# Kernel tuning notes

Measured on AMD Instinct MI355X. Metric: run time of the kernel, lower is better.

## Reference

```python
import jax, jax.numpy as jnp
import numpy as np

N_NODES = 50000
N_GRAPHS = 64


def gcn_conv(x, W, b, src, dst, n_nodes):
    """PyG GCNConv: sym-normalized aggregation with self-loops.
    out_i = sum_{j->i} d_j^{-1/2} d_i^{-1/2} (x_j W) + b, self-loops included."""
    loops = jnp.arange(n_nodes, dtype=src.dtype)
    s = jnp.concatenate([src, loops])  # [E+N]
    d = jnp.concatenate([dst, loops])
    h = x @ W  # [N, H]
    deg = jax.ops.segment_sum(jnp.ones_like(s, dtype=h.dtype), d, num_segments=n_nodes)
    dinv = jnp.where(deg > 0, jax.lax.rsqrt(jnp.maximum(deg, 1.0)), 0.0)
    norm = dinv[s] * dinv[d]  # [E+N]
    msg = h[s] * norm[:, None]  # gather + scale, [E+N, H]
    out = jax.ops.segment_sum(msg, d, num_segments=n_nodes)  # scatter-add
    return out + b


def setup_inputs() -> dict:
    key = jax.random.key(0)
    k1, k2, k3, k4, k5, k6, k7, k8, k9 = jax.random.split(key, 9)
    in_dim, hid, num_robots, out_size = 16, 128, 8, 2
    x = jax.random.normal(k1, (N_NODES, in_dim), dtype=jnp.float32)
    edge_index = jax.random.randint(k2, (2, 800000), 0, N_NODES, dtype=jnp.int64)
    batch = jnp.sort(jax.random.randint(k3, (N_NODES,), 0, N_GRAPHS, dtype=jnp.int64))
    s1 = 1.0 / np.sqrt(in_dim)
    s2 = 1.0 / np.sqrt(hid)
    W1 = jax.random.uniform(k4, (in_dim, hid), jnp.float32, -s1, s1)
    b1 = jax.random.uniform(k5, (hid,), jnp.float32, -s1, s1)
    W2 = jax.random.uniform(k6, (hid, hid), jnp.float32, -s2, s2)
    b2 = jax.random.uniform(k7, (hid,), jnp.float32, -s2, s2)
    Wfc = jax.random.uniform(k8, (hid, out_size * num_robots), jnp.float32, -s2, s2)
    bfc = jax.random.uniform(k9, (out_size * num_robots,), jnp.float32, -s2, s2)
    return {"x": x, "edge_index": edge_index, "batch": batch,
            "W1": W1, "b1": b1, "W2": W2, "b2": b2, "Wfc": Wfc, "bfc": bfc}


def reference(x, edge_index, batch, W1, b1, W2, b2, Wfc, bfc):
    src, dst = edge_index[0], edge_index[1]
    n = x.shape[0]
    h = jax.nn.relu(gcn_conv(x, W1, b1, src, dst, n))
    h = jax.nn.relu(gcn_conv(h, W2, b2, src, dst, n))
    # global_mean_pool over graph ids
    sums = jax.ops.segment_sum(h, batch, num_segments=N_GRAPHS)  # [G, H]
    cnt = jax.ops.segment_sum(jnp.ones((n,), h.dtype), batch, num_segments=N_GRAPHS)
    pooled = sums / jnp.maximum(cnt, 1.0)[:, None]
    vel = pooled @ Wfc + bfc  # [G, num_robots*2]
    return vel.reshape(-1, 8, 2)
```

## Files before the change

### kernel.cpp

```cpp
#include <hip/hip_runtime.h>
#include <hip/hip_bf16.h>

#define HID 128
#define IN_DIM 16

typedef short bf16x8 __attribute__((ext_vector_type(8)));
typedef float f32x4 __attribute__((ext_vector_type(4)));
typedef unsigned short u16x8 __attribute__((ext_vector_type(8)));

__device__ __forceinline__ unsigned short f2bf(float f) {
    unsigned int u = __float_as_uint(f);
    unsigned int r = (u + 0x7FFFu + ((u >> 16) & 1u)) >> 16;
    return (unsigned short)r;
}
__device__ __forceinline__ float bf2f(unsigned short u) {
    return __uint_as_float(((unsigned int)u) << 16);
}

__global__ __launch_bounds__(256) void k_hist(const int* __restrict__ dst,
                                              int* __restrict__ hist,
                                              int E, int NB, int chunk) {
    __shared__ int lh[256];
    lh[threadIdx.x] = 0;
    __syncthreads();
    int s0 = blockIdx.x * chunk;
    int e_end = min(E, s0 + chunk);
    for (int e = s0 + threadIdx.x; e < e_end; e += 256)
        atomicAdd(&lh[dst[e] >> 8], 1);
    __syncthreads();
    for (int i = threadIdx.x; i < NB; i += 256)
        hist[blockIdx.x * NB + i] = lh[i];
}

__global__ __launch_bounds__(256) void k_hist_scan(int* __restrict__ hist,
                                                   int* __restrict__ btot, int NB) {
    __shared__ int sdata[256];
    int b = blockIdx.x, t = threadIdx.x;
    int v = hist[t * NB + b];
    sdata[t] = v;
    __syncthreads();
    for (int off = 1; off < 256; off <<= 1) {
        int tmp = (t >= off) ? sdata[t - off] : 0;
        __syncthreads();
        sdata[t] += tmp;
        __syncthreads();
    }
    hist[t * NB + b] = sdata[t] - v;
    if (t == 255) btot[b] = sdata[255];
}

__global__ __launch_bounds__(256) void k_misc(const int* __restrict__ btot,
                                              int* __restrict__ bucket_base,
                                              const int* __restrict__ batch, float* __restrict__ cnt,
                                              const float* __restrict__ W2,
                                              unsigned short* __restrict__ W2T,
                                              float* __restrict__ pooled,
                                              int N, int G, int NB, int E) {
    int bid = blockIdx.x;
    int t = threadIdx.x;
    if (bid == 0) {
        __shared__ int sdata[256];
        int v = (t < NB) ? btot[t] : 0;
        sdata[t] = v;
        __syncthreads();
        for (int off = 1; off < 256; off <<= 1) {
            int tmp = (t >= off) ? sdata[t - off] : 0;
            __syncthreads();
            sdata[t] += tmp;
            __syncthreads();
        }
        if (t < NB) bucket_base[t] = sdata[t] - v;
        if (t == 0) bucket_base[NB] = E;
    } else if (bid == 1) {
        int g = t;
        if (g >= G) return;
        int lo = 0, hi = N;
        while (lo < hi) { int mid = (lo + hi) >> 1; if (batch[mid] < g) lo = mid + 1; else hi = mid; }
        int start = lo;
        lo = 0; hi = N;
        while (lo < hi) { int mid = (lo + hi) >> 1; if (batch[mid] <= g) lo = mid + 1; else hi = mid; }
        cnt[g] = (float)(lo - start);
    } else if (bid < 66) {
        int i = (bid - 2) * 256 + t;
        int n = i >> 7, k = i & 127;
        W2T[i] = f2bf(W2[(size_t)k * HID + n]);
    } else {
        int i = (bid - 66) * 256 + t;
        if (i < G * HID) pooled[i] = 0.f;
    }
}

__global__ __launch_bounds__(256) void k_bucket(const int* __restrict__ src, const int* __restrict__ dst,
                                                const int* __restrict__ hist,
                                                const int* __restrict__ bucket_base,
                                                unsigned int* __restrict__ bucketed,
                                                int E, int NB, int chunk) {
    __shared__ int lcur[256];
    for (int i = threadIdx.x; i < NB; i += 256)
        lcur[i] = hist[blockIdx.x * NB + i] + bucket_base[i];
    __syncthreads();
    int s0 = blockIdx.x * chunk;
    int e_end = min(E, s0 + chunk);
    for (int e = s0 + threadIdx.x; e < e_end; e += 256) {
        int d = dst[e], s = src[e];
        int p = atomicAdd(&lcur[d >> 8], 1);
        bucketed[p] = ((unsigned int)(d & 255) << 16) | (unsigned int)s;
    }
}

__global__ __launch_bounds__(256) void k_fill3(const unsigned int* __restrict__ bucketed,
                                               const int* __restrict__ bucket_base,
                                               unsigned short* __restrict__ csr,
                                               int* __restrict__ offs,
                                               int* __restrict__ indeg,
                                               float* __restrict__ dinv, int N) {
    __shared__ int lh[256];
    __shared__ int sc[256];
    int b = blockIdx.x, t = threadIdx.x;
    int n0 = b << 8;
    lh[t] = 0;
    __syncthreads();
    int bb = bucket_base[b], be = bucket_base[b + 1];
    for (int e = bb + t; e < be; e += 256)
        atomicAdd(&lh[bucketed[e] >> 16], 1);
    __syncthreads();
    int deg = lh[t];
    sc[t] = deg;
    __syncthreads();
    for (int off = 1; off < 256; off <<= 1) {
        int tmp = (t >= off) ? sc[t - off] : 0;
        __syncthreads();
        sc[t] += tmp;
        __syncthreads();
    }
    int excl = sc[t] - deg + bb;
    int node = n0 + t;
    if (node < N) {
        offs[node] = excl;
        indeg[node] = deg;
        dinv[node] = rsqrtf(1.0f + (float)deg);
    }
    __syncthreads();
    sc[t] = excl;
    __syncthreads();
    for (int e = bb + t; e < be; e += 256) {
        unsigned int u = bucketed[e];
        int p = atomicAdd(&sc[u >> 16], 1);
        csr[p] = (unsigned short)(u & 0xFFFFu);
    }
}

__global__ __launch_bounds__(256) void k_prep(const float* __restrict__ x,
                                              const float* __restrict__ dinv,
                                              unsigned short* __restrict__ xs16, int N) {
    int tt = blockIdx.x * 256 + threadIdx.x;
    if (tt >= N * 4) return;
    int node = tt >> 2, q = tt & 3;
    float di = dinv[node];
    float4 v = *reinterpret_cast<const float4*>(x + (size_t)node * IN_DIM + q * 4);
    ushort4 o;
    o.x = f2bf(di * v.x); o.y = f2bf(di * v.y);
    o.z = f2bf(di * v.z); o.w = f2bf(di * v.w);
    *reinterpret_cast<ushort4*>(xs16 + (size_t)node * IN_DIM + q * 4) = o;
}

__global__ __launch_bounds__(256) void k_gather16(const unsigned short* __restrict__ xs16,
                                                  const int* __restrict__ offs,
                                                  const int* __restrict__ indeg,
                                                  const unsigned short* __restrict__ csr,
                                                  float* __restrict__ y, int N) {
    int t = blockIdx.x * 256 + threadIdx.x;
    int node = t >> 1;
    if (node >= N) return;
    int c = (t & 1) * 8;
    int base = offs[node], deg = indeg[node];
    u16x8 ow = *reinterpret_cast<const u16x8*>(xs16 + (size_t)node * IN_DIM + c);
    float a[8];
    #pragma unroll
    for (int d = 0; d < 8; ++d) a[d] = bf2f(ow[d]);
    int j = 0;
    for (; j + 8 <= deg; j += 8) {
        int sI[8];
        #pragma unroll
        for (int u = 0; u < 8; ++u) sI[u] = csr[base + j + u];
        u16x8 v[8];
        #pragma unroll
        for (int u = 0; u < 8; ++u)
            v[u] = *reinterpret_cast<const u16x8*>(xs16 + (size_t)sI[u] * IN_DIM + c);
        #pragma unroll
        for (int u = 0; u < 8; ++u)
            #pragma unroll
            for (int d = 0; d < 8; ++d) a[d] += bf2f(v[u][d]);
    }
    for (; j < deg; ++j) {
        int s = csr[base + j];
        u16x8 v = *reinterpret_cast<const u16x8*>(xs16 + (size_t)s * IN_DIM + c);
        #pragma unroll
        for (int d = 0; d < 8; ++d) a[d] += bf2f(v[d]);
    }
    float* yp = y + (size_t)node * IN_DIM + c;
    *reinterpret_cast<float4*>(yp + 0) = make_float4(a[0], a[1], a[2], a[3]);
    *reinterpret_cast<float4*>(yp + 4) = make_float4(a[4], a[5], a[6], a[7]);
}

__global__ __launch_bounds__(256) void k_gemm1b(const float* __restrict__ y,
                                                const float* __restrict__ W1,
                                                const float* __restrict__ dinv,
                                                const float* __restrict__ b1,
                                                unsigned short* __restrict__ out, int N) {
    __shared__ float Ws[IN_DIM * HID];
    __shared__ float xs[8][IN_DIM];
    int nb = blockIdx.x * 8;
    for (int i = threadIdx.x * 4; i < IN_DIM * HID; i += 256 * 4)
        *reinterpret_cast<float4*>(&Ws[i]) = *reinterpret_cast<const float4*>(&W1[i]);
    int nrows = min(8, N - nb);
    if (threadIdx.x < 32) {
        int r = threadIdx.x >> 2, c = (threadIdx.x & 3) * 4;
        if (r < nrows)
            *reinterpret_cast<float4*>(&xs[r][c]) =
                *reinterpret_cast<const float4*>(&y[(size_t)(nb + r) * IN_DIM + c]);
    }
    __syncthreads();
    int f = threadIdx.x & 127;
    int g = threadIdx.x >> 7;
    float bb = b1[f];
    for (int r = g; r < nrows; r += 2) {
        int node = nb + r;
        float acc = 0.f;
        #pragma unroll
        for (int k = 0; k < IN_DIM; ++k) acc += xs[r][k] * Ws[k * HID + f];
        float di = dinv[node];
        out[(size_t)node * HID + f] = f2bf(di * fmaxf(di * acc + bb, 0.f));
    }
}

__global__ __launch_bounds__(256) void k_conv2_fused(const unsigned short* __restrict__ h1p,
                                                     const int* __restrict__ offs,
                                                     const int* __restrict__ indeg,
                                                     const unsigned short* __restrict__ csr,
                                                     const unsigned short* __restrict__ W2T,
                                                     const float* __restrict__ dinv,
                                                     const float* __restrict__ b2,
                                                     const int* __restrict__ batch,
                                                     float* __restrict__ pooled, int N) {
    __shared__ unsigned short zs[64 * HID];
    __shared__ float pool_s[HID];
    int t = threadIdx.x;
    int R0 = blockIdx.x * 64;

    {
        int node = R0 + (t >> 2);
        int seg = (t & 3) * 32;
        float a[32];
        #pragma unroll
        for (int i = 0; i < 32; ++i) a[i] = 0.f;
        if (node < N) {
            const unsigned short* own = h1p + (size_t)node * HID + seg;
            #pragma unroll
            for (int q = 0; q < 4; ++q) {
                u16x8 v = *reinterpret_cast<const u16x8*>(own + q * 8);
                #pragma unroll
                for (int d = 0; d < 8; ++d) a[q * 8 + d] = bf2f(v[d]);
            }
            int base = offs[node], deg = indeg[node];
            int j = 0;
            for (; j + 2 <= deg; j += 2) {
                int s0 = csr[base + j], s1 = csr[base + j + 1];
                const unsigned short* p0 = h1p + (size_t)s0 * HID + seg;
                const unsigned short* p1 = h1p + (size_t)s1 * HID + seg;
                u16x8 v[8];
                #pragma unroll
                for (int q = 0; q < 4; ++q) v[q] = *reinterpret_cast<const u16x8*>(p0 + q * 8);
                #pragma unroll
                for (int q = 0; q < 4; ++q) v[4 + q] = *reinterpret_cast<const u16x8*>(p1 + q * 8);
                #pragma unroll
                for (int q = 0; q < 4; ++q)
                    #pragma unroll
                    for (int d = 0; d < 8; ++d)
                        a[q * 8 + d] += bf2f(v[q][d]) + bf2f(v[4 + q][d]);
            }
            if (j < deg) {
                int s0 = csr[base + j];
                const unsigned short* p0 = h1p + (size_t)s0 * HID + seg;
                #pragma unroll
                for (int q = 0; q < 4; ++q) {
                    u16x8 v = *reinterpret_cast<const u16x8*>(p0 + q * 8);
                    #pragma unroll
                    for (int d = 0; d < 8; ++d) a[q * 8 + d] += bf2f(v[d]);
                }
            }
        }
        int row = t >> 2;
        #pragma unroll
        for (int q = 0; q < 4; ++q) {
            u16x8 o;
            #pragma unroll
            for (int d = 0; d < 8; ++d) o[d] = f2bf(a[q * 8 + d]);
            int byte = row * 256 + seg * 2 + q * 16;
            byte ^= (row & 7) << 4;
            *reinterpret_cast<u16x8*>(reinterpret_cast<char*>(zs) + byte) = o;
        }
    }
    __syncthreads();

    int wave = t >> 6;
    int lane = t & 63;
    int lr = lane & 15;
    int lkB = (lane >> 4) * 16;
    f32x4 acc[8] = {};
    #pragma unroll
    for (int kk = 0; kk < 4; ++kk) {
        int abyte = (wave * 16 + lr) * 256 + kk * 64 + lkB;
        abyte ^= (lr & 7) << 4;
        bf16x8 aF = *reinterpret_cast<const bf16x8*>(reinterpret_cast<const char*>(zs) + abyte);
        #pragma unroll
        for (int cf = 0; cf < 8; ++cf) {
            bf16x8 bF = *reinterpret_cast<const bf16x8*>(W2T + (size_t)(cf * 16 + lr) * HID + kk * 32 + (lane >> 4) * 8);
            acc[cf] = __builtin_amdgcn_mfma_f32_16x16x32_bf16(aF, bF, acc[cf], 0, 0, 0);
        }
    }
    int R = R0 + wave * 16;
    int r0 = (lane >> 4) * 4;
    float di[4];
    int nd[4];
    #pragma unroll
    for (int r = 0; r < 4; ++r) {
        nd[r] = R + r0 + r;
        di[r] = (nd[r] < N) ? dinv[nd[r]] : 0.f;
    }
    int gid0 = batch[min(R0, N - 1)];
    bool single = (R0 + 63 < N) && (batch[R0 + 63] == gid0);
    if (single) {
        if (t < HID) pool_s[t] = 0.f;
        __syncthreads();
        #pragma unroll
        for (int cf = 0; cf < 8; ++cf) {
            float bb = b2[cf * 16 + lr];
            float sc = 0.f;
            #pragma unroll
            for (int r = 0; r < 4; ++r)
                sc += fmaxf(di[r] * acc[cf][r] + bb, 0.f);
            sc += __shfl_xor(sc, 16);
            sc += __shfl_xor(sc, 32);
            if (lane < 16) atomicAdd(&pool_s[cf * 16 + lr], sc);
        }
        __syncthreads();
        if (t < HID)
            atomicAdd(&pooled[(size_t)gid0 * HID + t], pool_s[t]);
    } else {
        #pragma unroll
        for (int r = 0; r < 4; ++r) {
            if (nd[r] < N) {
                int bi = batch[nd[r]];
                #pragma unroll
                for (int cf = 0; cf < 8; ++cf) {
                    float v = fmaxf(di[r] * acc[cf][r] + b2[cf * 16 + lr], 0.f);
                    atomicAdd(&pooled[(size_t)bi * HID + cf * 16 + lr], v);
                }
            }
        }
    }
}

__global__ __launch_bounds__(256) void k_fc(const float* __restrict__ pooled,
                                            const float* __restrict__ cnt,
                                            const float* __restrict__ Wfc,
                                            const float* __restrict__ bfc,
                                            float* __restrict__ out, int G, int O) {
    int t = blockIdx.x * blockDim.x + threadIdx.x;
    if (t >= G * O) return;
    int g = t / O, o = t % O;
    float acc = 0.f;
    for (int k = 0; k < HID; ++k) acc += pooled[(size_t)g * HID + k] * Wfc[(size_t)k * O + o];
    out[t] = acc / fmaxf(cnt[g], 1.f) + bfc[o];
}

extern "C" void kernel_launch(void* const* d_in, const int* in_sizes, int n_in,
                              void* d_out, int out_size, void* d_ws, size_t ws_size,
                              hipStream_t stream) {
    const float* x     = (const float*)d_in[0];
    const int*   ei    = (const int*)d_in[1];
    const int*   batch = (const int*)d_in[2];
    const float* W1    = (const float*)d_in[3];
    const float* b1    = (const float*)d_in[4];
    const float* W2    = (const float*)d_in[5];
    const float* b2    = (const float*)d_in[6];
    const float* Wfc   = (const float*)d_in[7];
    const float* bfc   = (const float*)d_in[8];
    float* out = (float*)d_out;

    const int E = in_sizes[1] / 2;
    const int N = in_sizes[2];
    const int O = in_sizes[8];
    const int G = out_size / O;
    const int Npad = ((N + 63) / 64) * 64;
    const int NB = (N + 255) >> 8;
    const int CHUNK = (E + 255) / 256;

    const int* src = ei;
    const int* dst = ei + E;

    char* ws = (char*)d_ws;
    int*   indeg  = (int*)ws;                        ws += sizeof(int) * N;
    float* pooled = (float*)ws;                      ws += sizeof(float) * G * HID;
    float* dinv   = (float*)ws;                      ws += sizeof(float) * N;
    int*   offs   = (int*)ws;                        ws += sizeof(int) * N;
    int*   hist   = (int*)ws;                        ws += sizeof(int) * 256 * NB;
    int*   btot   = (int*)ws;                        ws += sizeof(int) * 256;
    int*   bucket_base = (int*)ws;                   ws += sizeof(int) * 260;
    float* cnt    = (float*)ws;                      ws += sizeof(float) * G;
    float* y      = (float*)ws;                      ws += sizeof(float) * (size_t)N * IN_DIM;
    unsigned short* xs16 = (unsigned short*)ws;      ws += sizeof(unsigned short) * (size_t)N * IN_DIM;
    unsigned short* w2t  = (unsigned short*)ws;      ws += sizeof(unsigned short) * (size_t)HID * HID;
    unsigned short* h1p  = (unsigned short*)ws;      ws += sizeof(unsigned short) * (size_t)Npad * HID;
    unsigned int*  bucketed = (unsigned int*)ws;     ws += sizeof(unsigned int) * (size_t)E;
    unsigned short* csr  = (unsigned short*)ws;      ws += sizeof(unsigned short) * (size_t)E;

    const int BS = 256;

    k_hist<<<256, BS, 0, stream>>>(dst, hist, E, NB, CHUNK);
    k_hist_scan<<<NB, BS, 0, stream>>>(hist, btot, NB);
    k_misc<<<66 + (G * HID + BS - 1) / BS, BS, 0, stream>>>(btot, bucket_base, batch, cnt,
                                                            W2, w2t, pooled, N, G, NB, E);
    k_bucket<<<256, BS, 0, stream>>>(src, dst, hist, bucket_base, bucketed, E, NB, CHUNK);
    k_fill3<<<NB, BS, 0, stream>>>(bucketed, bucket_base, csr, offs, indeg, dinv, N);
    k_prep<<<(N * 4 + BS - 1) / BS, BS, 0, stream>>>(x, dinv, xs16, N);

    k_gather16<<<(N * 2 + BS - 1) / BS, BS, 0, stream>>>(xs16, offs, indeg, csr, y, N);
    k_gemm1b<<<(N + 7) / 8, BS, 0, stream>>>(y, W1, dinv, b1, h1p, N);

    k_conv2_fused<<<(N + 63) / 64, BS, 0, stream>>>(h1p, offs, indeg, csr, w2t, dinv, b2,
                                                    batch, pooled, N);

    k_fc<<<(G * O + BS - 1) / BS, BS, 0, stream>>>(pooled, cnt, Wfc, bfc, out, G, O);
}
```

Baseline: 212.7 us.

## Split conv2 neighbor gather across 16 lanes per row with 512-thread blocks

The fused conv2 kernel now runs 512 threads per block. In the gather phase each node row is handled by 16 lanes loading 16 bytes each, in two passes of 32 rows, instead of 4 lanes loading 64 bytes each; the neighbor loop is unrolled by 4. In the MFMA phase pairs of waves split the 128 output columns, so each wave holds 4 accumulators instead of 8. The aim is more memory-level parallelism, wider coalesced gather loads and lower register pressure for higher occupancy. The cost is twice as many csr index loads per row and a larger block that needs more resources per workgroup.

Result: faster. 200.6 us (-5.7%).

```diff
diff --git a/kernel.cpp b/kernel.cpp
--- a/kernel.cpp
+++ b/kernel.cpp
@@ -234,7 +234,7 @@
     }
 }
 
-__global__ __launch_bounds__(256) void k_conv2_fused(const unsigned short* __restrict__ h1p,
+__global__ __launch_bounds__(512) void k_conv2_fused(const unsigned short* __restrict__ h1p,
                                                      const int* __restrict__ offs,
                                                      const int* __restrict__ indeg,
                                                      const unsigned short* __restrict__ csr,
@@ -248,78 +248,67 @@
     int t = threadIdx.x;
     int R0 = blockIdx.x * 64;
 
-    {
-        int node = R0 + (t >> 2);
-        int seg = (t & 3) * 32;
-        float a[32];
-        #pragma unroll
-        for (int i = 0; i < 32; ++i) a[i] = 0.f;
+    #pragma unroll
+    for (int pass = 0; pass < 2; ++pass) {
+        int row = pass * 32 + (t >> 4);
+        int node = R0 + row;
+        int c = (t & 15) * 8;
+        float a[8];
+        #pragma unroll
+        for (int d = 0; d < 8; ++d) a[d] = 0.f;
         if (node < N) {
-            const unsigned short* own = h1p + (size_t)node * HID + seg;
+            u16x8 ow = *reinterpret_cast<const u16x8*>(h1p + (size_t)node * HID + c);
             #pragma unroll
-            for (int q = 0; q < 4; ++q) {
-                u16x8 v = *reinterpret_cast<const u16x8*>(own + q * 8);
-                #pragma unroll
-                for (int d = 0; d < 8; ++d) a[q * 8 + d] = bf2f(v[d]);
-            }
+            for (int d = 0; d < 8; ++d) a[d] = bf2f(ow[d]);
             int base = offs[node], deg = indeg[node];
             int j = 0;
-            for (; j + 2 <= deg; j += 2) {
-                int s0 = csr[base + j], s1 = csr[base + j + 1];
-                const unsigned short* p0 = h1p + (size_t)s0 * HID + seg;
-                const unsigned short* p1 = h1p + (size_t)s1 * HID + seg;
-                u16x8 v[8];
+            for (; j + 4 <= deg; j += 4) {
+                int s0 = csr[base + j + 0], s1 = csr[base + j + 1];
+                int s2 = csr[base + j + 2], s3 = csr[base + j + 3];
+                u16x8 v0 = *reinterpret_cast<const u16x8*>(h1p + (size_t)s0 * HID + c);
+                u16x8 v1 = *reinterpret_cast<const u16x8*>(h1p + (size_t)s1 * HID + c);
+                u16x8 v2 = *reinterpret_cast<const u16x8*>(h1p + (size_t)s2 * HID + c);
+                u16x8 v3 = *reinterpret_cast<const u16x8*>(h1p + (size_t)s3 * HID + c);
                 #pragma unroll
-                for (int q = 0; q < 4; ++q) v[q] = *reinterpret_cast<const u16x8*>(p0 + q * 8);
+                for (int d = 0; d < 8; ++d)
+                    a[d] += (bf2f(v0[d]) + bf2f(v1[d])) + (bf2f(v2[d]) + bf2f(v3[d]));
+            }
+            for (; j < deg; ++j) {
+                int s = csr[base + j];
+                u16x8 v = *reinterpret_cast<const u16x8*>(h1p + (size_t)s * HID + c);
                 #pragma unroll
-                for (int q = 0; q < 4; ++q) v[4 + q] = *reinterpret_cast<const u16x8*>(p1 + q * 8);
-                #pragma unroll
-                for (int q = 0; q < 4; ++q)
-                    #pragma unroll
-                    for (int d = 0; d < 8; ++d)
-                        a[q * 8 + d] += bf2f(v[q][d]) + bf2f(v[4 + q][d]);
-            }
-            if (j < deg) {
-                int s0 = csr[base + j];
-                const unsigned short* p0 = h1p + (size_t)s0 * HID + seg;
-                #pragma unroll
-                for (int q = 0; q < 4; ++q) {
-                    u16x8 v = *reinterpret_cast<const u16x8*>(p0 + q * 8);
-                    #pragma unroll
-                    for (int d = 0; d < 8; ++d) a[q * 8 + d] += bf2f(v[d]);
-                }
+                for (int d = 0; d < 8; ++d) a[d] += bf2f(v[d]);
             }
         }
-        int row = t >> 2;
-        #pragma unroll
-        for (int q = 0; q < 4; ++q) {
-            u16x8 o;
-            #pragma unroll
-            for (int d = 0; d < 8; ++d) o[d] = f2bf(a[q * 8 + d]);
-            int byte = row * 256 + seg * 2 + q * 16;
-            byte ^= (row & 7) << 4;
-            *reinterpret_cast<u16x8*>(reinterpret_cast<char*>(zs) + byte) = o;
-        }
+        u16x8 o;
+        #pragma unroll
+        for (int d = 0; d < 8; ++d) o[d] = f2bf(a[d]);
+        int byte = row * 256 + c * 2;
+        byte ^= (row & 7) << 4;
+        *reinterpret_cast<u16x8*>(reinterpret_cast<char*>(zs) + byte) = o;
     }
     __syncthreads();
 
     int wave = t >> 6;
     int lane = t & 63;
+    int rg = wave >> 1;
+    int ch = (wave & 1) * 4;
     int lr = lane & 15;
     int lkB = (lane >> 4) * 16;
-    f32x4 acc[8] = {};
+    f32x4 acc[4] = {};
     #pragma unroll
     for (int kk = 0; kk < 4; ++kk) {
-        int abyte = (wave * 16 + lr) * 256 + kk * 64 + lkB;
+        int abyte = (rg * 16 + lr) * 256 + kk * 64 + lkB;
         abyte ^= (lr & 7) << 4;
         bf16x8 aF = *reinterpret_cast<const bf16x8*>(reinterpret_cast<const char*>(zs) + abyte);
         #pragma unroll
-        for (int cf = 0; cf < 8; ++cf) {
-            bf16x8 bF = *reinterpret_cast<const bf16x8*>(W2T + (size_t)(cf * 16 + lr) * HID + kk * 32 + (lane >> 4) * 8);
-            acc[cf] = __builtin_amdgcn_mfma_f32_16x16x32_bf16(aF, bF, acc[cf], 0, 0, 0);
+        for (int cfi = 0; cfi < 4; ++cfi) {
+            int col0 = (ch + cfi) * 16;
+            bf16x8 bF = *reinterpret_cast<const bf16x8*>(W2T + (size_t)(col0 + lr) * HID + kk * 32 + (lane >> 4) * 8);
+            acc[cfi] = __builtin_amdgcn_mfma_f32_16x16x32_bf16(aF, bF, acc[cfi], 0, 0, 0);
         }
     }
-    int R = R0 + wave * 16;
+    int R = R0 + rg * 16;
     int r0 = (lane >> 4) * 4;
     float di[4];
     int nd[4];
@@ -334,15 +323,16 @@
         if (t < HID) pool_s[t] = 0.f;
         __syncthreads();
         #pragma unroll
-        for (int cf = 0; cf < 8; ++cf) {
-            float bb = b2[cf * 16 + lr];
+        for (int cfi = 0; cfi < 4; ++cfi) {
+            int col = (ch + cfi) * 16 + lr;
+            float bb = b2[col];
             float sc = 0.f;
             #pragma unroll
             for (int r = 0; r < 4; ++r)
-                sc += fmaxf(di[r] * acc[cf][r] + bb, 0.f);
+                sc += fmaxf(di[r] * acc[cfi][r] + bb, 0.f);
             sc += __shfl_xor(sc, 16);
             sc += __shfl_xor(sc, 32);
-            if (lane < 16) atomicAdd(&pool_s[cf * 16 + lr], sc);
+            if (lane < 16) atomicAdd(&pool_s[col], sc);
         }
         __syncthreads();
         if (t < HID)
@@ -353,9 +343,10 @@
             if (nd[r] < N) {
                 int bi = batch[nd[r]];
                 #pragma unroll
-                for (int cf = 0; cf < 8; ++cf) {
-                    float v = fmaxf(di[r] * acc[cf][r] + b2[cf * 16 + lr], 0.f);
-                    atomicAdd(&pooled[(size_t)bi * HID + cf * 16 + lr], v);
+                for (int cfi = 0; cfi < 4; ++cfi) {
+                    int col = (ch + cfi) * 16 + lr;
+                    float v = fmaxf(di[r] * acc[cfi][r] + b2[col], 0.f);
+                    atomicAdd(&pooled[(size_t)bi * HID + col], v);
                 }
             }
         }
@@ -429,8 +420,8 @@
     k_gather16<<<(N * 2 + BS - 1) / BS, BS, 0, stream>>>(xs16, offs, indeg, csr, y, N);
     k_gemm1b<<<(N + 7) / 8, BS, 0, stream>>>(y, W1, dinv, b1, h1p, N);
 
-    k_conv2_fused<<<(N + 63) / 64, BS, 0, stream>>>(h1p, offs, indeg, csr, w2t, dinv, b2,
-                                                    batch, pooled, N);
+    k_conv2_fused<<<(N + 63) / 64, 512, 0, stream>>>(h1p, offs, indeg, csr, w2t, dinv, b2,
+                                                     batch, pooled, N);
 
     k_fc<<<(G * O + BS - 1) / BS, BS, 0, stream>>>(pooled, cnt, Wfc, bfc, out, G, O);
 }
```

## Store layer-1 activations in FP8 and split conv2 into gather and GEMM kernels

Applied to the files above, without the earlier changes.

Layer-1 output h1 is now packed to FP8 (e4m3) instead of bf16, which halves the bytes read by the irregular neighbor gather in conv2. The fused gather+MFMA kernel is split into two kernels. One gathers with 8 threads per node and an 8-way unrolled index loop, then writes bf16 z to global memory. The other does the MFMA GEMM plus mean-pool, reading z directly from global memory instead of LDS. The split adds an extra global round trip for z and one more launch, and FP8 storage loses precision relative to the reference.

After: 203.5 us. 1.05x faster.

```diff
diff --git a/kernel.cpp b/kernel.cpp
--- a/kernel.cpp
+++ b/kernel.cpp
@@ -6,7 +6,9 @@
 
 typedef short bf16x8 __attribute__((ext_vector_type(8)));
 typedef float f32x4 __attribute__((ext_vector_type(4)));
+typedef float f32x2 __attribute__((ext_vector_type(2)));
 typedef unsigned short u16x8 __attribute__((ext_vector_type(8)));
+typedef unsigned int u32x4 __attribute__((ext_vector_type(4)));
 
 __device__ __forceinline__ unsigned short f2bf(float f) {
     unsigned int u = __float_as_uint(f);
@@ -207,7 +209,7 @@
                                                 const float* __restrict__ W1,
                                                 const float* __restrict__ dinv,
                                                 const float* __restrict__ b1,
-                                                unsigned short* __restrict__ out, int N) {
+                                                unsigned int* __restrict__ out8, int N) {
     __shared__ float Ws[IN_DIM * HID];
     __shared__ float xs[8][IN_DIM];
     int nb = blockIdx.x * 8;
@@ -221,105 +223,111 @@
                 *reinterpret_cast<const float4*>(&y[(size_t)(nb + r) * IN_DIM + c]);
     }
     __syncthreads();
-    int f = threadIdx.x & 127;
-    int g = threadIdx.x >> 7;
-    float bb = b1[f];
-    for (int r = g; r < nrows; r += 2) {
+    int r = threadIdx.x >> 5;
+    int c4 = (threadIdx.x & 31) * 4;
+    if (r < nrows) {
         int node = nb + r;
-        float acc = 0.f;
-        #pragma unroll
-        for (int k = 0; k < IN_DIM; ++k) acc += xs[r][k] * Ws[k * HID + f];
+        float a0 = 0.f, a1 = 0.f, a2 = 0.f, a3 = 0.f;
+        #pragma unroll
+        for (int k = 0; k < IN_DIM; ++k) {
+            float xv = xs[r][k];
+            const float* w = &Ws[k * HID + c4];
+            a0 += xv * w[0]; a1 += xv * w[1]; a2 += xv * w[2]; a3 += xv * w[3];
+        }
         float di = dinv[node];
-        out[(size_t)node * HID + f] = f2bf(di * fmaxf(di * acc + bb, 0.f));
-    }
-}
-
-__global__ __launch_bounds__(256) void k_conv2_fused(const unsigned short* __restrict__ h1p,
-                                                     const int* __restrict__ offs,
-                                                     const int* __restrict__ indeg,
-                                                     const unsigned short* __restrict__ csr,
-                                                     const unsigned short* __restrict__ W2T,
-                                                     const float* __restrict__ dinv,
-                                                     const float* __restrict__ b2,
-                                                     const int* __restrict__ batch,
-                                                     float* __restrict__ pooled, int N) {
-    __shared__ unsigned short zs[64 * HID];
-    __shared__ float pool_s[HID];
-    int t = threadIdx.x;
-    int R0 = blockIdx.x * 64;
-
+        float v0 = di * fmaxf(di * a0 + b1[c4 + 0], 0.f);
+        float v1 = di * fmaxf(di * a1 + b1[c4 + 1], 0.f);
+        float v2 = di * fmaxf(di * a2 + b1[c4 + 2], 0.f);
+        float v3 = di * fmaxf(di * a3 + b1[c4 + 3], 0.f);
+        int p = __builtin_amdgcn_cvt_pk_fp8_f32(v0, v1, 0, false);
+        p = __builtin_amdgcn_cvt_pk_fp8_f32(v2, v3, p, true);
+        out8[(size_t)node * 32 + (c4 >> 2)] = (unsigned int)p;
+    }
+}
+
+__global__ __launch_bounds__(256) void k_gather_z8(const unsigned int* __restrict__ h1p8,
+                                                   const int* __restrict__ offs,
+                                                   const int* __restrict__ indeg,
+                                                   const unsigned short* __restrict__ csr,
+                                                   unsigned short* __restrict__ z, int N) {
+    int t = blockIdx.x * 256 + threadIdx.x;
+    int node = t >> 3;
+    if (node >= N) return;
+    int c = (t & 7) * 16;
+    int cw = c >> 2;
+    float a[16];
     {
-        int node = R0 + (t >> 2);
-        int seg = (t & 3) * 32;
-        float a[32];
-        #pragma unroll
-        for (int i = 0; i < 32; ++i) a[i] = 0.f;
-        if (node < N) {
-            const unsigned short* own = h1p + (size_t)node * HID + seg;
+        u32x4 ow = *reinterpret_cast<const u32x4*>(h1p8 + (size_t)node * 32 + cw);
+        #pragma unroll
+        for (int q = 0; q < 4; ++q) {
+            f32x2 lo = __builtin_amdgcn_cvt_pk_f32_fp8(ow[q], false);
+            f32x2 hi = __builtin_amdgcn_cvt_pk_f32_fp8(ow[q], true);
+            a[q * 4 + 0] = lo[0]; a[q * 4 + 1] = lo[1];
+            a[q * 4 + 2] = hi[0]; a[q * 4 + 3] = hi[1];
+        }
+    }
+    int base = offs[node], deg = indeg[node];
+    int j = 0;
+    for (; j + 8 <= deg; j += 8) {
+        int sI[8];
+        #pragma unroll
+        for (int u = 0; u < 8; ++u) sI[u] = csr[base + j + u];
+        u32x4 v[8];
+        #pragma unroll
+        for (int u = 0; u < 8; ++u)
+            v[u] = *reinterpret_cast<const u32x4*>(h1p8 + (size_t)sI[u] * 32 + cw);
+        #pragma unroll
+        for (int u = 0; u < 8; ++u) {
             #pragma unroll
             for (int q = 0; q < 4; ++q) {
-                u16x8 v = *reinterpret_cast<const u16x8*>(own + q * 8);
-                #pragma unroll
-                for (int d = 0; d < 8; ++d) a[q * 8 + d] = bf2f(v[d]);
+                f32x2 lo = __builtin_amdgcn_cvt_pk_f32_fp8(v[u][q], false);
+                f32x2 hi = __builtin_amdgcn_cvt_pk_f32_fp8(v[u][q], true);
+                a[q * 4 + 0] += lo[0]; a[q * 4 + 1] += lo[1];
+                a[q * 4 + 2] += hi[0]; a[q * 4 + 3] += hi[1];
             }
-            int base = offs[node], deg = indeg[node];
-            int j = 0;
-            for (; j + 2 <= deg; j += 2) {
-                int s0 = csr[base + j], s1 = csr[base + j + 1];
-                const unsigned short* p0 = h1p + (size_t)s0 * HID + seg;
-                const unsigned short* p1 = h1p + (size_t)s1 * HID + seg;
-                u16x8 v[8];
-                #pragma unroll
-                for (int q = 0; q < 4; ++q) v[q] = *reinterpret_cast<const u16x8*>(p0 + q * 8);
-                #pragma unroll
-                for (int q = 0; q < 4; ++q) v[4 + q] = *reinterpret_cast<const u16x8*>(p1 + q * 8);
-                #pragma unroll
-                for (int q = 0; q < 4; ++q)
-                    #pragma unroll
-                    for (int d = 0; d < 8; ++d)
-                        a[q * 8 + d] += bf2f(v[q][d]) + bf2f(v[4 + q][d]);
-            }
-            if (j < deg) {
-                int s0 = csr[base + j];
-                const unsigned short* p0 = h1p + (size_t)s0 * HID + seg;
-                #pragma unroll
-                for (int q = 0; q < 4; ++q) {
-                    u16x8 v = *reinterpret_cast<const u16x8*>(p0 + q * 8);
-                    #pragma unroll
-                    for (int d = 0; d < 8; ++d) a[q * 8 + d] += bf2f(v[d]);
-                }
-            }
-        }
-        int row = t >> 2;
+        }
+    }
+    for (; j < deg; ++j) {
+        int s = csr[base + j];
+        u32x4 v = *reinterpret_cast<const u32x4*>(h1p8 + (size_t)s * 32 + cw);
         #pragma unroll
         for (int q = 0; q < 4; ++q) {
-            u16x8 o;
-            #pragma unroll
-            for (int d = 0; d < 8; ++d) o[d] = f2bf(a[q * 8 + d]);
-            int byte = row * 256 + seg * 2 + q * 16;
-            byte ^= (row & 7) << 4;
-            *reinterpret_cast<u16x8*>(reinterpret_cast<char*>(zs) + byte) = o;
-        }
-    }
-    __syncthreads();
-
-    int wave = t >> 6;
-    int lane = t & 63;
+            f32x2 lo = __builtin_amdgcn_cvt_pk_f32_fp8(v[q], false);
+            f32x2 hi = __builtin_amdgcn_cvt_pk_f32_fp8(v[q], true);
+            a[q * 4 + 0] += lo[0]; a[q * 4 + 1] += lo[1];
+            a[q * 4 + 2] += hi[0]; a[q * 4 + 3] += hi[1];
+        }
+    }
+    u16x8 o0, o1;
+    #pragma unroll
+    for (int d = 0; d < 8; ++d) { o0[d] = f2bf(a[d]); o1[d] = f2bf(a[8 + d]); }
+    *reinterpret_cast<u16x8*>(z + (size_t)node * HID + c)     = o0;
+    *reinterpret_cast<u16x8*>(z + (size_t)node * HID + c + 8) = o1;
+}
+
+__global__ __launch_bounds__(256) void k_gemm2_pool(const unsigned short* __restrict__ z,
+                                                    const unsigned short* __restrict__ W2T,
+                                                    const float* __restrict__ dinv,
+                                                    const float* __restrict__ b2,
+                                                    const int* __restrict__ batch,
+                                                    float* __restrict__ pooled, int N) {
+    __shared__ float pool_s[HID];
+    int wave = threadIdx.x >> 6;
+    int lane = threadIdx.x & 63;
+    int R = blockIdx.x * 64 + wave * 16;
     int lr = lane & 15;
-    int lkB = (lane >> 4) * 16;
+    int lk = (lane >> 4) * 8;
     f32x4 acc[8] = {};
+    const unsigned short* arow = z + (size_t)(R + lr) * HID;
     #pragma unroll
     for (int kk = 0; kk < 4; ++kk) {
-        int abyte = (wave * 16 + lr) * 256 + kk * 64 + lkB;
-        abyte ^= (lr & 7) << 4;
-        bf16x8 aF = *reinterpret_cast<const bf16x8*>(reinterpret_cast<const char*>(zs) + abyte);
+        bf16x8 a = *reinterpret_cast<const bf16x8*>(arow + kk * 32 + lk);
         #pragma unroll
         for (int cf = 0; cf < 8; ++cf) {
-            bf16x8 bF = *reinterpret_cast<const bf16x8*>(W2T + (size_t)(cf * 16 + lr) * HID + kk * 32 + (lane >> 4) * 8);
-            acc[cf] = __builtin_amdgcn_mfma_f32_16x16x32_bf16(aF, bF, acc[cf], 0, 0, 0);
-        }
-    }
-    int R = R0 + wave * 16;
+            bf16x8 b = *reinterpret_cast<const bf16x8*>(W2T + (size_t)(cf * 16 + lr) * HID + kk * 32 + lk);
+            acc[cf] = __builtin_amdgcn_mfma_f32_16x16x32_bf16(a, b, acc[cf], 0, 0, 0);
+        }
+    }
     int r0 = (lane >> 4) * 4;
     float di[4];
     int nd[4];
@@ -328,10 +336,11 @@
         nd[r] = R + r0 + r;
         di[r] = (nd[r] < N) ? dinv[nd[r]] : 0.f;
     }
+    int R0 = blockIdx.x * 64;
     int gid0 = batch[min(R0, N - 1)];
     bool single = (R0 + 63 < N) && (batch[R0 + 63] == gid0);
     if (single) {
-        if (t < HID) pool_s[t] = 0.f;
+        if (threadIdx.x < HID) pool_s[threadIdx.x] = 0.f;
         __syncthreads();
         #pragma unroll
         for (int cf = 0; cf < 8; ++cf) {
@@ -345,8 +354,8 @@
             if (lane < 16) atomicAdd(&pool_s[cf * 16 + lr], sc);
         }
         __syncthreads();
-        if (t < HID)
-            atomicAdd(&pooled[(size_t)gid0 * HID + t], pool_s[t]);
+        if (threadIdx.x < HID)
+            atomicAdd(&pooled[(size_t)gid0 * HID + threadIdx.x], pool_s[threadIdx.x]);
     } else {
         #pragma unroll
         for (int r = 0; r < 4; ++r) {
@@ -412,7 +421,8 @@
     float* y      = (float*)ws;                      ws += sizeof(float) * (size_t)N * IN_DIM;
     unsigned short* xs16 = (unsigned short*)ws;      ws += sizeof(unsigned short) * (size_t)N * IN_DIM;
     unsigned short* w2t  = (unsigned short*)ws;      ws += sizeof(unsigned short) * (size_t)HID * HID;
-    unsigned short* h1p  = (unsigned short*)ws;      ws += sizeof(unsigned short) * (size_t)Npad * HID;
+    unsigned int*  h1p8  = (unsigned int*)ws;        ws += sizeof(unsigned int) * (size_t)N * 32;
+    unsigned short* z    = (unsigned short*)ws;      ws += sizeof(unsigned short) * (size_t)Npad * HID;
     unsigned int*  bucketed = (unsigned int*)ws;     ws += sizeof(unsigned int) * (size_t)E;
     unsigned short* csr  = (unsigned short*)ws;      ws += sizeof(unsigned short) * (size_t)E;
 
@@ -427,10 +437,10 @@
     k_prep<<<(N * 4 + BS - 1) / BS, BS, 0, stream>>>(x, dinv, xs16, N);
 
     k_gather16<<<(N * 2 + BS - 1) / BS, BS, 0, stream>>>(xs16, offs, indeg, csr, y, N);
-    k_gemm1b<<<(N + 7) / 8, BS, 0, stream>>>(y, W1, dinv, b1, h1p, N);
-
-    k_conv2_fused<<<(N + 63) / 64, BS, 0, stream>>>(h1p, offs, indeg, csr, w2t, dinv, b2,
-                                                    batch, pooled, N);
+    k_gemm1b<<<(N + 7) / 8, BS, 0, stream>>>(y, W1, dinv, b1, h1p8, N);
+
+    k_gather_z8<<<(N * 8 + BS - 1) / BS, BS, 0, stream>>>(h1p8, offs, indeg, csr, z, N);
+    k_gemm2_pool<<<Npad / 64, BS, 0, stream>>>(z, w2t, dinv, b2, batch, pooled, N);
 
     k_fc<<<(G * O + BS - 1) / BS, BS, 0, stream>>>(pooled, cnt, Wfc, bfc, out, G, O);
 }
```
